# Kernel tuning notes

Measured on AMD Instinct MI355X. Metric: run time of the kernel, lower is better.

## Reference

```python
import jax, jax.numpy as jnp
import numpy as np
from jax import lax

H, W = 1024, 2048
WIN = (3, 3)            # eps=1.5 on the integer grid == 8-neighborhood (3x3 window)
MIN_SAMPLES = 4         # sklearn DBSCAN counts the point itself
MIN_CLUSTER = 30        # clusters smaller than this become noise
N_SLOTS = 26            # output channels
INT32_MAX = np.iinfo(np.int32).max


def setup_inputs() -> dict:
    key = jax.random.key(0)
    mask = jax.random.normal(key, (H, W), dtype=jnp.float32)
    return {"mask": mask}


def _minpool(x):
    # 3x3 min over int32 labels, SAME padding with +inf identity
    return lax.reduce_window(x, INT32_MAX, lax.min, WIN, (1, 1), 'SAME')


def _forward(mask):
    h, w = mask.shape
    hw = h * w
    BIG = jnp.int32(hw)  # sentinel label for 'not in any cluster'

    active = mask > 0.1
    # neighbor count in 3x3 (includes self) -> DBSCAN core condition
    cnt = lax.reduce_window(active.astype(jnp.int32), 0, lax.add, WIN, (1, 1), 'SAME')
    core = active & (cnt >= MIN_SAMPLES)

    idx2d = jnp.arange(hw, dtype=jnp.int32).reshape(h, w)
    L0 = jnp.where(core, idx2d, BIG)

    # connected components over core pixels: min-label hook (3x3 min-pool)
    # + pointer jumping (path compression) until fixpoint
    def body(st):
        L, _ = st
        Ln = jnp.where(core, jnp.minimum(L, _minpool(L)), BIG)
        flat = Ln.ravel()
        table = jnp.concatenate([flat, jnp.array([hw], jnp.int32)])  # BIG -> BIG
        flat = table[table[flat]]  # two pointer-jump hops
        Ln = flat.reshape(h, w)
        return Ln, jnp.all(Ln == L)

    def cond(st):
        return jnp.logical_not(st[1])

    L, _ = lax.while_loop(cond, body, (L0, jnp.array(False)))

    # border points: active non-core pixels with a core neighbor join the
    # (deterministically min-labeled) neighboring core cluster
    pooled = _minpool(L)
    final = jnp.where(core, L, jnp.where(active & (pooled < BIG), pooled, BIG))

    flatL = final.ravel()
    labeled = flatL < BIG
    ids = jnp.where(labeled, flatL, hw)  # noise -> extra bucket hw

    sizes = jax.ops.segment_sum(labeled.astype(jnp.int32), ids, num_segments=hw + 1)[:hw]
    col = jnp.broadcast_to(jnp.arange(w, dtype=jnp.float32), (h, w)).ravel()
    colsum = jax.ops.segment_sum(jnp.where(labeled, col, 0.0), ids, num_segments=hw + 1)[:hw]

    valid = sizes >= MIN_CLUSTER  # size filter (loc.sum() < 30 -> noise)
    means = jnp.where(valid, colsum / jnp.maximum(sizes, 1), jnp.inf)
    order = jnp.argsort(means)  # valid clusters first, sorted by mean column
    rank = jnp.zeros(hw, jnp.int32).at[order].set(jnp.arange(hw, dtype=jnp.int32))

    lab = jnp.where(labeled, flatL, 0)
    ch = rank[lab]
    pix_ok = labeled & valid[lab] & (ch < N_SLOTS)
    ch2d = jnp.where(pix_ok, ch, N_SLOTS).reshape(h, w)  # N_SLOTS == 'no channel'
    # scatter 1s into the rank-th channel
    return (ch2d[None] == jnp.arange(N_SLOTS, dtype=jnp.int32)[:, None, None]).astype(jnp.uint8)


def reference(mask):
    return _forward(mask)
```

## Files before the change

### kernel.cpp

```cpp
#include <hip/hip_runtime.h>
#include <stdint.h>

#define HH 1024
#define WW 2048
#define HWN (HH*WW)
#define BIGL HWN
#define NSLOTS 26
#define MINCL 30
#define THREADS 256
#define LTHREADS 512
#define MAXCAND 70000
#define HSZ 512
#define TILE 4096
#define NTILES 512
#define NB 128

typedef int vi4 __attribute__((ext_vector_type(4)));
typedef unsigned long long u64;

__device__ __forceinline__ int uf_load(int* p, int i) {
    return __hip_atomic_load(&p[i], __ATOMIC_RELAXED, __HIP_MEMORY_SCOPE_AGENT);
}
__device__ __forceinline__ void uf_store(int* p, int i, int v) {
    __hip_atomic_store(&p[i], v, __ATOMIC_RELAXED, __HIP_MEMORY_SCOPE_AGENT);
}
__device__ int uf_find(int* parent, int x) {
    int p = uf_load(parent, x);
    while (p != x) {
        int gp = uf_load(parent, p);
        if (gp != p) uf_store(parent, x, gp);
        x = p; p = gp;
    }
    return p;
}
__device__ void uf_union(int* parent, int a, int b) {
    int ra = uf_find(parent, a);
    int rb = uf_find(parent, b);
    while (ra != rb) {
        if (ra > rb) { int t = ra; ra = rb; rb = t; }
        int old = atomicCAS(&parent[rb], rb, ra);
        if (old == rb) return;
        rb = uf_find(parent, old);
        ra = uf_find(parent, ra);
    }
}

__device__ __forceinline__ int l_load(int* p, int i) {
    return __hip_atomic_load(&p[i], __ATOMIC_RELAXED, __HIP_MEMORY_SCOPE_WORKGROUP);
}
__device__ __forceinline__ void l_store(int* p, int i, int v) {
    __hip_atomic_store(&p[i], v, __ATOMIC_RELAXED, __HIP_MEMORY_SCOPE_WORKGROUP);
}
__device__ int l_find(int* lp, int x) {
    int p = l_load(lp, x);
    while (p != x) {
        int gp = l_load(lp, p);
        if (gp != p) l_store(lp, x, gp);
        x = p; p = gp;
    }
    return p;
}
__device__ void l_union(int* lp, int a, int b) {
    int ra = l_find(lp, a);
    int rb = l_find(lp, b);
    while (ra != rb) {
        if (ra > rb) { int t = ra; ra = rb; rb = t; }
        int old = atomicCAS(&lp[rb], rb, ra);
        if (old == rb) return;
        rb = l_find(lp, old);
        ra = l_find(lp, ra);
    }
}

__global__ __launch_bounds__(LTHREADS) void k_local(const float* __restrict__ mask,
                                                    uint8_t* __restrict__ flags,
                                                    int* __restrict__ parent,
                                                    int* __restrict__ sizes,
                                                    unsigned long long* __restrict__ colsum,
                                                    signed char* __restrict__ chan,
                                                    int* __restrict__ counter) {
    __shared__ uint8_t lact[66 * 72];
    __shared__ uint8_t lc8[TILE];
    __shared__ int lp[TILE];
    const int tid = threadIdx.x;
    int tile_x = blockIdx.x & 31, tile_y = blockIdx.x >> 5;
    int r0 = tile_y << 6, c0 = tile_x << 6;

    {
        int base = blockIdx.x * (HWN / NTILES);
        vi4* sz4 = (vi4*)(sizes + base);
        vi4* cs4 = (vi4*)(colsum + base);
        for (int t = tid; t < 1024; t += LTHREADS) sz4[t] = (vi4)0;
        for (int t = tid; t < 2048; t += LTHREADS) cs4[t] = (vi4)0;
        vi4* ch4 = (vi4*)(chan + base);
        for (int t = tid; t < 256; t += LTHREADS) ch4[t] = (vi4)(-1);
        if (blockIdx.x == 0 && tid == 0) { counter[0] = 0; counter[1] = 0; }
    }

    {
        int tx = tid & 15, ty = tid >> 4;
        for (int yy = ty; yy < 66; yy += 32) {
            int gr = r0 - 1 + yy;
            for (int xx = tx; xx < 66; xx += 16) {
                int gc = c0 - 1 + xx;
                bool a = false;
                if ((unsigned)gr < HH && (unsigned)gc < WW)
                    a = mask[gr * WW + gc] > 0.1f;
                lact[yy * 72 + xx] = a ? 1 : 0;
            }
        }
    }
    __syncthreads();
    for (int li = tid; li < TILE; li += LTHREADS) {
        int lr = li >> 6, lc = li & 63;
        int b = (lr + 1) * 72 + (lc + 1);
        int a = lact[b];
        int cnt = lact[b - 73] + lact[b - 72] + lact[b - 71]
                + lact[b - 1]  + a           + lact[b + 1]
                + lact[b + 71] + lact[b + 72] + lact[b + 73];
        lc8[li] = (uint8_t)(a | ((a && cnt >= 4) ? 2 : 0));
        lp[li] = li;
    }
    __syncthreads();
    if (tid < 256) {
        int row = tid >> 2, chunk = tid & 3;
        ((uint4*)(flags + (size_t)(r0 + row) * WW + c0))[chunk] =
            ((const uint4*)lc8)[row * 4 + chunk];
    }
    for (int li = tid; li < TILE; li += LTHREADS) {
        if (!(lc8[li] & 2)) continue;
        int lr = li >> 6, lc = li & 63;
        if (lc > 0 && (lc8[li - 1] & 2)) l_union(lp, li, li - 1);
        if (lr > 0) {
            if (lc > 0  && (lc8[li - 65] & 2)) l_union(lp, li, li - 65);
            if (           (lc8[li - 64] & 2)) l_union(lp, li, li - 64);
            if (lc < 63 && (lc8[li - 63] & 2)) l_union(lp, li, li - 63);
        }
    }
    __syncthreads();
    for (int li = tid; li < TILE; li += LTHREADS) {
        if (!(lc8[li] & 2)) continue;
        int root = li, p;
        while ((p = lp[root]) != root) root = p;
        int gi = (r0 + (li >> 6)) * WW + c0 + (li & 63);
        int gr = (r0 + (root >> 6)) * WW + c0 + (root & 63);
        parent[gi] = gr;
    }
}

__global__ __launch_bounds__(THREADS) void k_merge(const uint8_t* __restrict__ flags,
                                                   int* __restrict__ parent) {
    int tile_x = blockIdx.x & 31, tile_y = blockIdx.x >> 5;
    int r0 = tile_y << 6, c0 = tile_x << 6;
    int t = threadIdx.x;
    int lane = t & 63;

    if (t < 64) {
        int r = r0, c = c0 + t, i = r * WW + c;
        bool selfC = (flags[i] & 2) != 0;
        bool nC = false, nwC = false, neC = false;
        if (selfC && r > 0) {
            nC  = (flags[i - WW] & 2) != 0;
            nwC = (c > 0)      && (flags[i - WW - 1] & 2);
            neC = (c < WW - 1) && (flags[i - WW + 1] & 2);
        }
        int did = 0, ra = -1, rb = -1;
        if (selfC && r > 0 && nC) { ra = uf_find(parent, i); rb = uf_find(parent, i - WW); did = 1; }
        int pra = __shfl_up(ra, 1), prb = __shfl_up(rb, 1), pdid = __shfl_up(did, 1);
        bool head = (lane == 0) || !pdid || pra != ra || prb != rb;
        if (did && head) uf_union(parent, ra, rb);
        if (selfC && r > 0) {
            if (t == 0) {
                if (nwC) uf_union(parent, i, i - WW - 1);
                if (!nC && neC) uf_union(parent, i, i - WW + 1);
            } else if (t == 63) {
                if (!nC && nwC) uf_union(parent, i, i - WW - 1);
                if (neC) {
                    bool eC = (c < WW - 1) && (flags[i + 1] & 2);
                    if (!eC) uf_union(parent, i, i - WW + 1);
                }
            } else if (!nC) {
                if (nwC) uf_union(parent, i, i - WW - 1);
                if (neC) uf_union(parent, i, i - WW + 1);
            }
        }
        if (t == 0 && selfC && c > 0 && (flags[i - 1] & 2))
            uf_union(parent, i, i - 1);
    } else if (t < 127) {
        int lr = t - 63;
        int r = r0 + lr, c = c0, i = r * WW + c;
        bool selfC = (flags[i] & 2) != 0;
        bool wC = false, nwC = false;
        if (selfC && c > 0) {
            wC  = (flags[i - 1] & 2) != 0;
            nwC = (flags[i - WW - 1] & 2) != 0;
        }
        int did = 0, ra = -1, rb = -1;
        if (selfC && wC) { ra = uf_find(parent, i); rb = uf_find(parent, i - 1); did = 1; }
        int pra = __shfl_up(ra, 1), prb = __shfl_up(rb, 1), pdid = __shfl_up(did, 1);
        bool head = (lane == 0) || !pdid || pra != ra || prb != rb;
        if (did && head) uf_union(parent, ra, rb);
        if (selfC && !wC && nwC) uf_union(parent, i, i - WW - 1);
    } else if (t < 190) {
        int lr = t - 126;
        int r = r0 + lr, c = c0 + 63, i = r * WW + c;
        bool selfC = (flags[i] & 2) != 0;
        if (selfC && c < WW - 1) {
            bool neC = (flags[i - WW + 1] & 2) != 0;
            bool eC  = (flags[i + 1] & 2) != 0;
            if (neC && !eC) uf_union(parent, i, i - WW + 1);
        }
    }
}

__global__ __launch_bounds__(THREADS) void k_border_stats(
        const uint8_t* __restrict__ flags, int* __restrict__ parent,
        int* __restrict__ labfull, int* __restrict__ sizes,
        unsigned long long* __restrict__ colsum,
        int* __restrict__ cand, int* __restrict__ counter) {
    __shared__ int h_lab[HSZ];
    __shared__ int h_sz[HSZ];
    __shared__ unsigned long long h_cs[HSZ];
    for (int t = threadIdx.x; t < HSZ; t += THREADS) {
        h_lab[t] = -1; h_sz[t] = 0; h_cs[t] = 0;
    }
    __syncthreads();

    int i = blockIdx.x * THREADS + threadIdx.x;
    int f = flags[i];
    int lab = BIGL;
    if (f & 2) {
        lab = uf_find(parent, i);
    } else if (f & 1) {
        int r = i >> 11, c = i & (WW - 1);
        int m = BIGL;
        #pragma unroll
        for (int dr = -1; dr <= 1; ++dr) {
            int rr = r + dr;
            if (rr < 0 || rr >= HH) continue;
            #pragma unroll
            for (int dc = -1; dc <= 1; ++dc) {
                int cc = c + dc;
                if (cc < 0 || cc >= WW) continue;
                int n = rr * WW + cc;
                if (flags[n] & 2) {
                    int v = uf_find(parent, n);
                    if (v < m) m = v;
                }
            }
        }
        lab = m;
    }
    labfull[i] = lab;

    int lane = threadIdx.x & 63;
    int labp = __shfl_up(lab, 1);
    bool head = (lane == 0) || (labp != lab);
    unsigned long long hm = __ballot(head);
    if (head && lab < BIGL) {
        unsigned long long rest = (hm >> lane) >> 1;
        int len = rest ? __ffsll((unsigned long long)rest) : (64 - lane);
        long long c0 = (long long)(i & (WW - 1));
        unsigned long long csum =
            (unsigned long long)(c0 * len + (long long)len * (len - 1) / 2);
        unsigned slot = (((unsigned)lab * 2654435761u) >> 20) & (HSZ - 1);
        for (;;) {
            int old = atomicCAS(&h_lab[slot], -1, lab);
            if (old == -1 || old == lab) {
                atomicAdd(&h_sz[slot], len);
                atomicAdd(&h_cs[slot], csum);
                break;
            }
            slot = (slot + 1) & (HSZ - 1);
        }
    }
    __syncthreads();
    for (int t = threadIdx.x; t < HSZ; t += THREADS) {
        int lb = h_lab[t];
        if (lb >= 0) {
            int add = h_sz[t];
            int old = atomicAdd(&sizes[lb], add);
            if (old < MINCL && old + add >= MINCL) {
                int p = atomicAdd(counter, 1);
                cand[p] = lb;
            }
            atomicAdd(&colsum[lb], h_cs[t]);
        }
    }
}

__device__ __forceinline__ u64 wave_min_u64(u64 m) {
    #pragma unroll
    for (int off = 32; off; off >>= 1) {
        u64 o = __shfl_xor(m, off);
        if (o < m) m = o;
    }
    return m;
}

__global__ __launch_bounds__(THREADS) void k_sel(const int* __restrict__ cand,
                                                 int* __restrict__ counter,
                                                 const int* __restrict__ sizes,
                                                 const unsigned long long* __restrict__ colsum,
                                                 unsigned long long* __restrict__ top26g,
                                                 signed char* __restrict__ chan) {
    __shared__ u64 wout[4 * NSLOTS];
    const int tid = threadIdx.x, lane = tid & 63, wv = tid >> 6;
    const int n = counter[0];
    int slice = (n + NB - 1) / NB;
    int j0 = blockIdx.x * slice;
    int j1 = j0 + slice; if (j1 > n) j1 = n;
    int len = j1 - j0; if (len < 0) len = 0;
    int chunk = (len + 3) >> 2;
    int s0 = j0 + wv * chunk;
    int s1 = s0 + chunk; if (s1 > j1) s1 = j1;

    u64 kk[3] = { ~0ull, ~0ull, ~0ull };
    #pragma unroll
    for (int t = 0; t < 3; ++t) {
        int j = s0 + lane + 64 * t;
        if (j < s1) {
            int lab = cand[j];
            float mean = (float)colsum[lab] / (float)sizes[lab];
            kk[t] = ((u64)__float_as_uint(mean) << 32) | (unsigned)lab;
        }
    }
    for (int k = 0; k < NSLOTS; ++k) {
        u64 m = kk[0]; int li = 0;
        if (kk[1] < m) { m = kk[1]; li = 1; }
        if (kk[2] < m) { m = kk[2]; li = 2; }
        u64 mpre = m;
        m = wave_min_u64(m);
        if (mpre == m && m != ~0ull) kk[li] = ~0ull;
        if (lane == 0) wout[wv * NSLOTS + k] = m;
    }
    __syncthreads();
    if (wv == 0) {
        u64 a = (lane < 4 * NSLOTS) ? wout[lane] : ~0ull;
        u64 b = (lane + 64 < 4 * NSLOTS) ? wout[lane + 64] : ~0ull;
        for (int k = 0; k < NSLOTS; ++k) {
            u64 m = a < b ? a : b; int li = a < b ? 0 : 1;
            u64 mpre = m;
            m = wave_min_u64(m);
            if (mpre == m && m != ~0ull) { if (li == 0) a = ~0ull; else b = ~0ull; }
            if (lane == 0) top26g[blockIdx.x * NSLOTS + k] = m;
        }
    }
    __syncthreads();
    __shared__ int lastflag;
    if (tid == 0) {
        __threadfence();
        lastflag = (atomicAdd(&counter[1], 1) == NB - 1);
    }
    __syncthreads();
    if (!lastflag) return;

    u64 mk[13];
    #pragma unroll
    for (int t = 0; t < 13; ++t) {
        int j = wv * 832 + lane + 64 * t;
        mk[t] = __hip_atomic_load(&top26g[j], __ATOMIC_RELAXED, __HIP_MEMORY_SCOPE_AGENT);
    }
    for (int k = 0; k < NSLOTS; ++k) {
        u64 m = mk[0]; int li = 0;
        #pragma unroll
        for (int t = 1; t < 13; ++t) if (mk[t] < m) { m = mk[t]; li = t; }
        u64 mpre = m;
        m = wave_min_u64(m);
        if (mpre == m && m != ~0ull) mk[li] = ~0ull;
        if (lane == 0) wout[wv * NSLOTS + k] = m;
    }
    __syncthreads();
    if (wv == 0) {
        u64 a = (lane < 4 * NSLOTS) ? wout[lane] : ~0ull;
        u64 b = (lane + 64 < 4 * NSLOTS) ? wout[lane + 64] : ~0ull;
        for (int k = 0; k < NSLOTS; ++k) {
            u64 m = a < b ? a : b; int li = a < b ? 0 : 1;
            u64 mpre = m;
            m = wave_min_u64(m);
            if (mpre == m && m != ~0ull) { if (li == 0) a = ~0ull; else b = ~0ull; }
            if (lane == 0 && m != ~0ull)
                chan[(unsigned int)(m & 0xFFFFFFFFull)] = (signed char)k;
        }
    }
}

__global__ __launch_bounds__(THREADS) void k_output(const int* __restrict__ labfull,
                                                    const signed char* __restrict__ chan,
                                                    int* __restrict__ out) {
    int i4 = (blockIdx.x * THREADS + threadIdx.x) * 4;
    int chv[4];
    #pragma unroll
    for (int t = 0; t < 4; ++t) {
        int lab = labfull[i4 + t];
        chv[t] = (lab < BIGL) ? (int)chan[lab] : -1;
    }
    #pragma unroll
    for (int c = 0; c < NSLOTS; ++c) {
        vi4 v;
        v.x = (chv[0] == c) ? 1 : 0;
        v.y = (chv[1] == c) ? 1 : 0;
        v.z = (chv[2] == c) ? 1 : 0;
        v.w = (chv[3] == c) ? 1 : 0;
        __builtin_nontemporal_store(v, (vi4*)(out + (size_t)c * HWN + i4));
    }
}

extern "C" void kernel_launch(void* const* d_in, const int* in_sizes, int n_in,
                              void* d_out, int out_size, void* d_ws, size_t ws_size,
                              hipStream_t stream) {
    const float* mask = (const float*)d_in[0];
    int* out = (int*)d_out;

    char* w = (char*)d_ws;
    int* parent                 = (int*)(w);
    int* labfull                = (int*)(w + (size_t)HWN * 4);
    int* sizes                  = (int*)(w + (size_t)HWN * 8);
    unsigned long long* colsum  = (unsigned long long*)(w + (size_t)HWN * 12);
    uint8_t* flags              = (uint8_t*)(w + (size_t)HWN * 20);
    signed char* chan           = (signed char*)(w + (size_t)HWN * 21);
    int* cand                   = (int*)(w + (size_t)HWN * 22);
    int* counter                = (int*)(w + (size_t)HWN * 22 + MAXCAND * 4);
    unsigned long long* top26g  = (unsigned long long*)(w + (size_t)HWN * 22 + MAXCAND * 4 + 256);

    const int blocks = HWN / THREADS;
    k_local       <<<NTILES, LTHREADS, 0, stream>>>(mask, flags, parent,
                                                    sizes, colsum, chan, counter);
    k_merge       <<<NTILES, THREADS, 0, stream>>>(flags, parent);
    k_border_stats<<<blocks, THREADS, 0, stream>>>(flags, parent, labfull, sizes, colsum,
                                                   cand, counter);
    k_sel         <<<NB, THREADS, 0, stream>>>(cand, counter, sizes, colsum, top26g, chan);
    k_output      <<<HWN / (4 * THREADS), THREADS, 0, stream>>>(labfull, chan, out);
}
```

Measured before the change: 405.4 us.

## Vectorize mask tile load and dedupe union-find root lookups via shared hash

The tile halo load in the labeling kernel now reads the 64x64 interior with float4 loads and fills the one-pixel border with separate small loops, replacing scalar strided loads. In the border/stats kernel, each block first gathers the distinct parent pointers of its core pixels and their core neighbors into a shared hash table. It then runs uf_find once per distinct entry and has every pixel look up its root from that table. This is meant to cut redundant pointer-chasing global loads, at the cost of an extra hash insertion pass, extra shared memory, and two more barriers.

```diff
diff --git a/kernel.cpp b/kernel.cpp
--- a/kernel.cpp
+++ b/kernel.cpp
@@ -98,17 +98,40 @@
     }
 
     {
-        int tx = tid & 15, ty = tid >> 4;
-        for (int yy = ty; yy < 66; yy += 32) {
-            int gr = r0 - 1 + yy;
-            for (int xx = tx; xx < 66; xx += 16) {
-                int gc = c0 - 1 + xx;
-                bool a = false;
-                if ((unsigned)gr < HH && (unsigned)gc < WW)
-                    a = mask[gr * WW + gc] > 0.1f;
-                lact[yy * 72 + xx] = a ? 1 : 0;
-            }
-        }
+        int lr = tid >> 4, q = tid & 15;
+        #pragma unroll
+        for (int pass = 0; pass < 2; ++pass) {
+            int rr = lr + pass * 32;
+            const float4* src = (const float4*)(mask + (size_t)(r0 + rr) * WW + c0);
+            float4 v = src[q];
+            uint8_t* dst = &lact[(rr + 1) * 72 + (q * 4 + 1)];
+            dst[0] = v.x > 0.1f; dst[1] = v.y > 0.1f;
+            dst[2] = v.z > 0.1f; dst[3] = v.w > 0.1f;
+        }
+    }
+    if (tid < 32) {
+        int q = tid & 15;
+        bool top = tid < 16;
+        int gr = top ? r0 - 1 : r0 + 64;
+        int yy = top ? 0 : 65;
+        uint8_t* dst = &lact[yy * 72 + (q * 4 + 1)];
+        if ((unsigned)gr < HH) {
+            const float4* src = (const float4*)(mask + (size_t)gr * WW + c0);
+            float4 v = src[q];
+            dst[0] = v.x > 0.1f; dst[1] = v.y > 0.1f;
+            dst[2] = v.z > 0.1f; dst[3] = v.w > 0.1f;
+        } else {
+            dst[0] = 0; dst[1] = 0; dst[2] = 0; dst[3] = 0;
+        }
+    } else if (tid >= 64 && tid < 64 + 132) {
+        int lane = tid - 64;
+        int side = lane >= 66;
+        int yy = side ? lane - 66 : lane;
+        int gr = r0 - 1 + yy;
+        int gc = side ? c0 + 64 : c0 - 1;
+        bool a = false;
+        if ((unsigned)gr < HH && (unsigned)gc < WW) a = mask[(size_t)gr * WW + gc] > 0.1f;
+        lact[yy * 72 + (side ? 65 : 0)] = a ? 1 : 0;
     }
     __syncthreads();
     for (int li = tid; li < TILE; li += LTHREADS) {
@@ -213,42 +236,80 @@
     }
 }
 
+__device__ __forceinline__ void h_insert(int* h_key, int p) {
+    unsigned slot = (((unsigned)p * 2654435761u) >> 20) & (HSZ - 1);
+    for (;;) {
+        int old = atomicCAS(&h_key[slot], -1, p);
+        if (old == -1 || old == p) return;
+        slot = (slot + 1) & (HSZ - 1);
+    }
+}
+__device__ __forceinline__ int h_lookup(const int* h_key, const int* h_root, int p) {
+    unsigned slot = (((unsigned)p * 2654435761u) >> 20) & (HSZ - 1);
+    for (;;) {
+        if (h_key[slot] == p) return h_root[slot];
+        slot = (slot + 1) & (HSZ - 1);
+    }
+}
+
 __global__ __launch_bounds__(THREADS) void k_border_stats(
         const uint8_t* __restrict__ flags, int* __restrict__ parent,
         int* __restrict__ labfull, int* __restrict__ sizes,
         unsigned long long* __restrict__ colsum,
         int* __restrict__ cand, int* __restrict__ counter) {
-    __shared__ int h_lab[HSZ];
-    __shared__ int h_sz[HSZ];
-    __shared__ unsigned long long h_cs[HSZ];
+    __shared__ int h_key[HSZ];
+    __shared__ int h_root[HSZ];
+    __shared__ int s_lab[HSZ];
+    __shared__ int s_sz[HSZ];
+    __shared__ u64 s_cs[HSZ];
     for (int t = threadIdx.x; t < HSZ; t += THREADS) {
-        h_lab[t] = -1; h_sz[t] = 0; h_cs[t] = 0;
-    }
-    __syncthreads();
-
-    int i = blockIdx.x * THREADS + threadIdx.x;
-    int f = flags[i];
+        h_key[t] = -1; s_lab[t] = -1; s_sz[t] = 0; s_cs[t] = 0;
+    }
+    __syncthreads();
+
+    const int i = blockIdx.x * THREADS + threadIdx.x;
+    const int f = flags[i];
+    const int r = i >> 11, c = i & (WW - 1);
+
+    int pself = -1;
+    int pnb[8];
+    #pragma unroll
+    for (int t = 0; t < 8; ++t) pnb[t] = -1;
+
+    if (f & 2) {
+        pself = parent[i];
+        h_insert(h_key, pself);
+    } else if (f & 1) {
+        const int dr8[8] = {-1,-1,-1, 0,0, 1,1,1};
+        const int dc8[8] = {-1, 0, 1,-1,1,-1,0,1};
+        #pragma unroll
+        for (int t = 0; t < 8; ++t) {
+            int rr = r + dr8[t], cc = c + dc8[t];
+            if ((unsigned)rr < HH && (unsigned)cc < WW) {
+                int n = rr * WW + cc;
+                if (flags[n] & 2) {
+                    int p = parent[n];
+                    pnb[t] = p;
+                    h_insert(h_key, p);
+                }
+            }
+        }
+    }
+    __syncthreads();
+    for (int t = threadIdx.x; t < HSZ; t += THREADS) {
+        int k = h_key[t];
+        if (k >= 0) h_root[t] = uf_find(parent, k);
+    }
+    __syncthreads();
+
     int lab = BIGL;
     if (f & 2) {
-        lab = uf_find(parent, i);
+        lab = h_lookup(h_key, h_root, pself);
     } else if (f & 1) {
-        int r = i >> 11, c = i & (WW - 1);
         int m = BIGL;
         #pragma unroll
-        for (int dr = -1; dr <= 1; ++dr) {
-            int rr = r + dr;
-            if (rr < 0 || rr >= HH) continue;
-            #pragma unroll
-            for (int dc = -1; dc <= 1; ++dc) {
-                int cc = c + dc;
-                if (cc < 0 || cc >= WW) continue;
-                int n = rr * WW + cc;
-                if (flags[n] & 2) {
-                    int v = uf_find(parent, n);
-                    if (v < m) m = v;
-                }
-            }
-        }
+        for (int t = 0; t < 8; ++t)
+            if (pnb[t] >= 0) { int v = h_lookup(h_key, h_root, pnb[t]); if (v < m) m = v; }
         lab = m;
     }
     labfull[i] = lab;
@@ -260,15 +321,14 @@
     if (head && lab < BIGL) {
         unsigned long long rest = (hm >> lane) >> 1;
         int len = rest ? __ffsll((unsigned long long)rest) : (64 - lane);
-        long long c0 = (long long)(i & (WW - 1));
-        unsigned long long csum =
-            (unsigned long long)(c0 * len + (long long)len * (len - 1) / 2);
+        long long cc0 = (long long)(i & (WW - 1));
+        u64 csum = (u64)(cc0 * len + (long long)len * (len - 1) / 2);
         unsigned slot = (((unsigned)lab * 2654435761u) >> 20) & (HSZ - 1);
         for (;;) {
-            int old = atomicCAS(&h_lab[slot], -1, lab);
+            int old = atomicCAS(&s_lab[slot], -1, lab);
             if (old == -1 || old == lab) {
-                atomicAdd(&h_sz[slot], len);
-                atomicAdd(&h_cs[slot], csum);
+                atomicAdd(&s_sz[slot], len);
+                atomicAdd(&s_cs[slot], csum);
                 break;
             }
             slot = (slot + 1) & (HSZ - 1);
@@ -276,15 +336,15 @@
     }
     __syncthreads();
     for (int t = threadIdx.x; t < HSZ; t += THREADS) {
-        int lb = h_lab[t];
+        int lb = s_lab[t];
         if (lb >= 0) {
-            int add = h_sz[t];
+            int add = s_sz[t];
             int old = atomicAdd(&sizes[lb], add);
             if (old < MINCL && old + add >= MINCL) {
                 int p = atomicAdd(counter, 1);
                 cand[p] = lb;
             }
-            atomicAdd(&colsum[lb], h_cs[t]);
+            atomicAdd(&colsum[lb], s_cs[t]);
         }
     }
 }
```

Result: faster. 388.1 us (-4.3%).
